# Optimization experiments

Measured on AMD Instinct MI355X. Metric: run time of the kernel, lower is better.

Reference implementation:

```python
import jax, jax.numpy as jnp
import numpy as np

N_NODES = 100000
N_EDGES = 3200000
IN_DIM = 512
HID_DIM = 16
OUT_DIM = 64


def _gcn_layer(E, X, W, b, n_nodes):
    # Standard GCN layer (CatGNN GCNLayer_MPNN_2):
    # add self-loops, symmetric deg^-1/2 normalization, project, gather-scatter sum.
    src = jnp.concatenate([E[0], jnp.arange(n_nodes, dtype=E.dtype)])
    dst = jnp.concatenate([E[1], jnp.arange(n_nodes, dtype=E.dtype)])
    deg = jax.ops.segment_sum(jnp.ones_like(dst, dtype=X.dtype), dst, num_segments=n_nodes)
    dinv = jnp.where(deg > 0, jax.lax.rsqrt(deg), 0.0)  # deg^-1/2, safe
    h = X @ W  # [N, d_out] project BEFORE aggregation (cheaper gather)
    norm = dinv[src] * dinv[dst]  # [E+N]
    msg = h[src] * norm[:, None]  # gather + scale
    out = jax.ops.segment_sum(msg, dst, num_segments=n_nodes)  # scatter-sum
    return out + b


def setup_inputs() -> dict:
    key = jax.random.key(0)
    k1, k2, k3, k4, k5 = jax.random.split(key, 5)
    V = jnp.arange(N_NODES, dtype=jnp.int64)
    E = jax.random.randint(k1, (2, N_EDGES), 0, N_NODES, dtype=jnp.int64)
    X = jax.random.normal(k2, (N_NODES, IN_DIM), dtype=jnp.float32)
    # Glorot-style init for layer weights
    W1 = jax.random.normal(k3, (IN_DIM, HID_DIM), dtype=jnp.float32) / np.sqrt(IN_DIM)
    b1 = jnp.zeros((HID_DIM,), dtype=jnp.float32)
    W2 = jax.random.normal(k4, (HID_DIM, OUT_DIM), dtype=jnp.float32) / np.sqrt(HID_DIM)
    b2 = jnp.zeros((OUT_DIM,), dtype=jnp.float32)
    return {"V": V, "E": E, "X": X, "W1": W1, "b1": b1, "W2": W2, "b2": b2}


def reference(V, E, X, W1, b1, W2, b2):
    n_nodes = V.shape[0]
    H = jax.nn.relu(_gcn_layer(E, X, W1, b1, n_nodes))
    # dropout is identity in eval mode
    H = _gcn_layer(E, H, W2, b2, n_nodes)
    return H
```

## Files before the change

kernel.cpp:

```cpp
#include <hip/hip_runtime.h>

#define HID 16
#define ODIM 64
#define IDIM 512
#define BKB 8
#define BKS 256
#define PTILE 4096
#define MAXBE 12288

__global__ __launch_bounds__(256) void k_bhist(const int* __restrict__ dst,
                                               int* __restrict__ bcnt, int ne, int nbk) {
    __shared__ int h[512];
    for (int t = threadIdx.x; t < 512; t += 256) h[t] = 0;
    __syncthreads();
    int stride = gridDim.x * blockDim.x;
    for (int e = blockIdx.x * blockDim.x + threadIdx.x; e < ne; e += stride)
        atomicAdd(&h[dst[e] >> BKB], 1);
    __syncthreads();
    for (int t = threadIdx.x; t < nbk; t += 256)
        if (h[t]) atomicAdd(&bcnt[t], h[t]);
}

__global__ __launch_bounds__(512) void k_bscan(const int* __restrict__ bcnt,
                                               int* __restrict__ bbase,
                                               int* __restrict__ bcur, int nbk) {
    __shared__ int s[512];
    int t = threadIdx.x;
    int v = (t < nbk) ? bcnt[t] : 0;
    s[t] = v;
    __syncthreads();
    for (int off = 1; off < 512; off <<= 1) {
        int u = (t >= off) ? s[t - off] : 0;
        __syncthreads();
        s[t] += u;
        __syncthreads();
    }
    if (t < nbk) { int b = s[t] - v; bbase[t] = b; bcur[t] = b; }
}

__global__ __launch_bounds__(512) void k_part(const int* __restrict__ src,
                                              const int* __restrict__ dst,
                                              int* __restrict__ bcur,
                                              unsigned int* __restrict__ ebuf,
                                              int ne, int nbk) {
    __shared__ int h[512], sc[512], base[512], lcur[512];
    __shared__ unsigned int sval[PTILE];
    __shared__ int saddr[PTILE];
    int e0 = blockIdx.x * PTILE;
    int m = ne - e0; if (m > PTILE) m = PTILE;
    if (m <= 0) return;
    int t = threadIdx.x;
    h[t] = 0;
    __syncthreads();
    for (int k = t; k < m; k += 512) atomicAdd(&h[dst[e0 + k] >> BKB], 1);
    __syncthreads();
    int hv = h[t];
    sc[t] = hv;
    __syncthreads();
    for (int off = 1; off < 512; off <<= 1) {
        int u = (t >= off) ? sc[t - off] : 0;
        __syncthreads();
        sc[t] += u;
        __syncthreads();
    }
    base[t] = hv ? atomicAdd(&bcur[t], hv) : 0;
    lcur[t] = 0;
    __syncthreads();
    for (int k = t; k < m; k += 512) {
        int d = dst[e0 + k];
        int b = d >> BKB;
        int r = atomicAdd(&lcur[b], 1);
        int slot = sc[b] - h[b] + r;
        sval[slot] = ((unsigned int)src[e0 + k] << BKB) | (unsigned int)(d & (BKS - 1));
        saddr[slot] = base[b] + r;
    }
    __syncthreads();
    for (int k = t; k < m; k += 512) ebuf[saddr[k]] = sval[k];
}

__global__ __launch_bounds__(256) void k_csr(const int* __restrict__ bbase,
                                             const int* __restrict__ bcnt,
                                             const unsigned int* __restrict__ ebuf,
                                             int* __restrict__ cnt,
                                             int* __restrict__ row_start,
                                             int* __restrict__ csr_src, int n) {
    __shared__ int h[256], sc[256], lc[256];
    __shared__ int stage[MAXBE];
    int bk = blockIdx.x;
    int node0 = bk << BKB;
    int ebase = bbase[bk];
    int ecnt = bcnt[bk];
    int t = threadIdx.x;
    h[t] = 0; lc[t] = 0;
    __syncthreads();
    for (int k = t; k < ecnt; k += 256) atomicAdd(&h[ebuf[ebase + k] & (BKS - 1)], 1);
    __syncthreads();
    int hv = h[t];
    sc[t] = hv;
    __syncthreads();
    for (int off = 1; off < 256; off <<= 1) {
        int u = (t >= off) ? sc[t - off] : 0;
        __syncthreads();
        sc[t] += u;
        __syncthreads();
    }
    int node = node0 + t;
    if (node < n) { cnt[node] = hv; row_start[node] = ebase + sc[t] - hv; }
    if (ecnt <= MAXBE) {
        for (int k = t; k < ecnt; k += 256) {
            unsigned int p = ebuf[ebase + k];
            int dl = p & (BKS - 1);
            int r = atomicAdd(&lc[dl], 1);
            stage[sc[dl] - h[dl] + r] = (int)(p >> BKB);
        }
        __syncthreads();
        for (int k = t; k < ecnt; k += 256) csr_src[ebase + k] = stage[k];
    } else {
        for (int k = t; k < ecnt; k += 256) {
            unsigned int p = ebuf[ebase + k];
            int dl = p & (BKS - 1);
            int r = atomicAdd(&lc[dl], 1);
            csr_src[ebase + sc[dl] - h[dl] + r] = (int)(p >> BKB);
        }
    }
}

__global__ __launch_bounds__(256) void k_proj1(const float* __restrict__ X,
                                               const float* __restrict__ W1,
                                               const int* __restrict__ cnt,
                                               float* __restrict__ hs1, int n) {
    __shared__ float Ws[IDIM * HID];
    for (int t = threadIdx.x; t < IDIM * HID; t += 256) Ws[t] = W1[t];
    __syncthreads();

    int i = blockIdx.x * blockDim.x + threadIdx.x;
    if (i >= n) return;

    const float4* xr = (const float4*)(X + (size_t)i * IDIM);
    float acc[HID];
#pragma unroll
    for (int j = 0; j < HID; ++j) acc[j] = 0.f;

    for (int k4 = 0; k4 < IDIM / 4; ++k4) {
        float4 x = xr[k4];
        const float* w = &Ws[k4 * 4 * HID];
#pragma unroll
        for (int j = 0; j < HID; ++j) acc[j] += x.x * w[j];
#pragma unroll
        for (int j = 0; j < HID; ++j) acc[j] += x.y * w[HID + j];
#pragma unroll
        for (int j = 0; j < HID; ++j) acc[j] += x.z * w[2 * HID + j];
#pragma unroll
        for (int j = 0; j < HID; ++j) acc[j] += x.w * w[3 * HID + j];
    }

    float di = rsqrtf((float)(cnt[i] + 1));
    float4* h4 = (float4*)(hs1 + (size_t)i * HID);
#pragma unroll
    for (int q = 0; q < 4; ++q) {
        float4 v;
        v.x = acc[q * 4 + 0] * di;
        v.y = acc[q * 4 + 1] * di;
        v.z = acc[q * 4 + 2] * di;
        v.w = acc[q * 4 + 3] * di;
        h4[q] = v;
    }
}

__global__ __launch_bounds__(256) void k_gather(const int* __restrict__ row_start,
                                                const int* __restrict__ cnt,
                                                const int* __restrict__ csr_src,
                                                const float* __restrict__ hs,
                                                float* __restrict__ agg, int n) {
    int tid = blockIdx.x * blockDim.x + threadIdx.x;
    int i = tid >> 2;
    int q = tid & 3;
    if (i >= n) return;
    int rs = row_start[i];
    int c = cnt[i];
    const float4* h4 = (const float4*)hs;
    float4 acc = h4[(size_t)i * 4 + q];
    int k = 0;
    for (; k + 1 < c; k += 2) {
        int s0 = csr_src[rs + k];
        int s1 = csr_src[rs + k + 1];
        float4 v0 = h4[(size_t)s0 * 4 + q];
        float4 v1 = h4[(size_t)s1 * 4 + q];
        acc.x += v0.x; acc.y += v0.y; acc.z += v0.z; acc.w += v0.w;
        acc.x += v1.x; acc.y += v1.y; acc.z += v1.z; acc.w += v1.w;
    }
    if (k < c) {
        int s0 = csr_src[rs + k];
        float4 v0 = h4[(size_t)s0 * 4 + q];
        acc.x += v0.x; acc.y += v0.y; acc.z += v0.z; acc.w += v0.w;
    }
    ((float4*)agg)[(size_t)i * 4 + q] = acc;
}

__global__ void k_mid(const int* __restrict__ cnt, const float* __restrict__ b1,
                      float* __restrict__ buf, int n) {
    int t = blockIdx.x * blockDim.x + threadIdx.x;
    if (t >= n * HID) return;
    int i = t >> 4;
    int j = t & 15;
    float di = rsqrtf((float)(cnt[i] + 1));
    float h = di * buf[t] + b1[j];
    h = fmaxf(h, 0.f);
    buf[t] = h * di;
}

__global__ __launch_bounds__(256) void k_out(const int* __restrict__ cnt,
                                             const float* __restrict__ agg2,
                                             const float* __restrict__ W2,
                                             const float* __restrict__ b2,
                                             float* __restrict__ out, int n) {
    __shared__ float Ws[HID * ODIM];
    __shared__ float bs[ODIM];
    for (int t = threadIdx.x; t < HID * ODIM; t += 256) Ws[t] = W2[t];
    if (threadIdx.x < ODIM) bs[threadIdx.x] = b2[threadIdx.x];
    __syncthreads();

    int t = blockIdx.x * blockDim.x + threadIdx.x;
    if (t >= n * ODIM) return;
    int i = t >> 6;
    int j = t & 63;
    float di = rsqrtf((float)(cnt[i] + 1));
    const float* g = agg2 + (size_t)i * HID;
    float acc = 0.f;
#pragma unroll
    for (int k = 0; k < HID; ++k) acc += g[k] * Ws[k * ODIM + j];
    out[t] = di * acc + bs[j];
}

extern "C" void kernel_launch(void* const* d_in, const int* in_sizes, int n_in,
                              void* d_out, int out_size, void* d_ws, size_t ws_size,
                              hipStream_t stream) {
    const int* E = (const int*)d_in[1];
    const float* X = (const float*)d_in[2];
    const float* W1 = (const float*)d_in[3];
    const float* b1 = (const float*)d_in[4];
    const float* W2 = (const float*)d_in[5];
    const float* b2 = (const float*)d_in[6];
    float* out = (float*)d_out;

    const int n = in_sizes[0];
    const int ne = in_sizes[1] / 2;
    const int* src = E;
    const int* dst = E + ne;
    const int nbk = (n + BKS - 1) >> BKB;

    char* ws = (char*)d_ws;
    int* bcnt = (int*)ws;
    int* bbase = (int*)(ws + (8u << 10));
    int* bcur = (int*)(ws + (16u << 10));
    int* cnt = (int*)(ws + (1u << 20));
    int* row_start = (int*)(ws + (2u << 20));
    unsigned int* ebuf = (unsigned int*)(ws + (3u << 20));
    float* B1 = (float*)(ws + (3u << 20));
    float* B2 = (float*)(ws + (10u << 20));
    int* csr_src = (int*)(ws + (17u << 20));

    hipMemsetAsync(bcnt, 0, nbk * sizeof(int), stream);
    k_bhist<<<1024, 256, 0, stream>>>(dst, bcnt, ne, nbk);
    k_bscan<<<1, 512, 0, stream>>>(bcnt, bbase, bcur, nbk);
    k_part<<<(ne + PTILE - 1) / PTILE, 512, 0, stream>>>(src, dst, bcur, ebuf, ne, nbk);
    k_csr<<<nbk, 256, 0, stream>>>(bbase, bcnt, ebuf, cnt, row_start, csr_src, n);

    k_proj1<<<(n + 255) / 256, 256, 0, stream>>>(X, W1, cnt, B1, n);
    k_gather<<<(n * 4 + 255) / 256, 256, 0, stream>>>(row_start, cnt, csr_src, B1, B2, n);
    k_mid<<<(n * HID + 255) / 256, 256, 0, stream>>>(cnt, b1, B2, n);
    k_gather<<<(n * 4 + 255) / 256, 256, 0, stream>>>(row_start, cnt, csr_src, B2, B1, n);
    k_out<<<(n * ODIM + 255) / 256, 256, 0, stream>>>(cnt, B1, W2, b2, out, n);
}
```

Baseline: 555.9 us.

## Drop CSR build; aggregate per bucket with LDS atomics and fuse epilogues

Removes the per-bucket CSR sort and instead computes only degrees, then aggregates each 256-node destination bucket directly from the bucketed edge buffer into shared memory using float atomics. The ReLU/bias/normalization step is fused into the first aggregation, and the W2 projection plus bias into the second. This eliminates the csr_src build and several separate elementwise kernels. The cost is heavy LDS atomic contention with nondeterministic summation order, and only about 391 blocks of 512 threads, which limits parallelism.

```diff
diff --git a/kernel.cpp b/kernel.cpp
--- a/kernel.cpp
+++ b/kernel.cpp
@@ -6,7 +6,6 @@
 #define BKB 8
 #define BKS 256
 #define PTILE 4096
-#define MAXBE 12288
 
 __global__ __launch_bounds__(256) void k_bhist(const int* __restrict__ dst,
                                                int* __restrict__ bcnt, int ne, int nbk) {
@@ -78,56 +77,25 @@
     for (int k = t; k < m; k += 512) ebuf[saddr[k]] = sval[k];
 }
 
-__global__ __launch_bounds__(256) void k_csr(const int* __restrict__ bbase,
+__global__ __launch_bounds__(256) void k_deg(const int* __restrict__ bbase,
                                              const int* __restrict__ bcnt,
                                              const unsigned int* __restrict__ ebuf,
-                                             int* __restrict__ cnt,
-                                             int* __restrict__ row_start,
-                                             int* __restrict__ csr_src, int n) {
-    __shared__ int h[256], sc[256], lc[256];
-    __shared__ int stage[MAXBE];
+                                             float* __restrict__ dinv, int n) {
+    __shared__ int h[BKS];
     int bk = blockIdx.x;
-    int node0 = bk << BKB;
-    int ebase = bbase[bk];
-    int ecnt = bcnt[bk];
-    int t = threadIdx.x;
-    h[t] = 0; lc[t] = 0;
-    __syncthreads();
-    for (int k = t; k < ecnt; k += 256) atomicAdd(&h[ebuf[ebase + k] & (BKS - 1)], 1);
-    __syncthreads();
-    int hv = h[t];
-    sc[t] = hv;
-    __syncthreads();
-    for (int off = 1; off < 256; off <<= 1) {
-        int u = (t >= off) ? sc[t - off] : 0;
-        __syncthreads();
-        sc[t] += u;
-        __syncthreads();
-    }
-    int node = node0 + t;
-    if (node < n) { cnt[node] = hv; row_start[node] = ebase + sc[t] - hv; }
-    if (ecnt <= MAXBE) {
-        for (int k = t; k < ecnt; k += 256) {
-            unsigned int p = ebuf[ebase + k];
-            int dl = p & (BKS - 1);
-            int r = atomicAdd(&lc[dl], 1);
-            stage[sc[dl] - h[dl] + r] = (int)(p >> BKB);
-        }
-        __syncthreads();
-        for (int k = t; k < ecnt; k += 256) csr_src[ebase + k] = stage[k];
-    } else {
-        for (int k = t; k < ecnt; k += 256) {
-            unsigned int p = ebuf[ebase + k];
-            int dl = p & (BKS - 1);
-            int r = atomicAdd(&lc[dl], 1);
-            csr_src[ebase + sc[dl] - h[dl] + r] = (int)(p >> BKB);
-        }
-    }
+    int t = threadIdx.x;
+    h[t] = 0;
+    __syncthreads();
+    int eb = bbase[bk], ec = bcnt[bk];
+    for (int k = t; k < ec; k += 256) atomicAdd(&h[ebuf[eb + k] & (BKS - 1)], 1);
+    __syncthreads();
+    int node = (bk << BKB) + t;
+    if (node < n) dinv[node] = rsqrtf((float)(h[t] + 1));
 }
 
 __global__ __launch_bounds__(256) void k_proj1(const float* __restrict__ X,
                                                const float* __restrict__ W1,
-                                               const int* __restrict__ cnt,
+                                               const float* __restrict__ dinv,
                                                float* __restrict__ hs1, int n) {
     __shared__ float Ws[IDIM * HID];
     for (int t = threadIdx.x; t < IDIM * HID; t += 256) Ws[t] = W1[t];
@@ -154,7 +122,7 @@
         for (int j = 0; j < HID; ++j) acc[j] += x.w * w[3 * HID + j];
     }
 
-    float di = rsqrtf((float)(cnt[i] + 1));
+    float di = dinv[i];
     float4* h4 = (float4*)(hs1 + (size_t)i * HID);
 #pragma unroll
     for (int q = 0; q < 4; ++q) {
@@ -167,69 +135,100 @@
     }
 }
 
-__global__ __launch_bounds__(256) void k_gather(const int* __restrict__ row_start,
-                                                const int* __restrict__ cnt,
-                                                const int* __restrict__ csr_src,
-                                                const float* __restrict__ hs,
-                                                float* __restrict__ agg, int n) {
-    int tid = blockIdx.x * blockDim.x + threadIdx.x;
-    int i = tid >> 2;
-    int q = tid & 3;
-    if (i >= n) return;
-    int rs = row_start[i];
-    int c = cnt[i];
-    const float4* h4 = (const float4*)hs;
-    float4 acc = h4[(size_t)i * 4 + q];
-    int k = 0;
-    for (; k + 1 < c; k += 2) {
-        int s0 = csr_src[rs + k];
-        int s1 = csr_src[rs + k + 1];
-        float4 v0 = h4[(size_t)s0 * 4 + q];
-        float4 v1 = h4[(size_t)s1 * 4 + q];
-        acc.x += v0.x; acc.y += v0.y; acc.z += v0.z; acc.w += v0.w;
-        acc.x += v1.x; acc.y += v1.y; acc.z += v1.z; acc.w += v1.w;
-    }
-    if (k < c) {
-        int s0 = csr_src[rs + k];
-        float4 v0 = h4[(size_t)s0 * 4 + q];
-        acc.x += v0.x; acc.y += v0.y; acc.z += v0.z; acc.w += v0.w;
-    }
-    ((float4*)agg)[(size_t)i * 4 + q] = acc;
-}
-
-__global__ void k_mid(const int* __restrict__ cnt, const float* __restrict__ b1,
-                      float* __restrict__ buf, int n) {
-    int t = blockIdx.x * blockDim.x + threadIdx.x;
-    if (t >= n * HID) return;
-    int i = t >> 4;
-    int j = t & 15;
-    float di = rsqrtf((float)(cnt[i] + 1));
-    float h = di * buf[t] + b1[j];
-    h = fmaxf(h, 0.f);
-    buf[t] = h * di;
-}
-
-__global__ __launch_bounds__(256) void k_out(const int* __restrict__ cnt,
-                                             const float* __restrict__ agg2,
-                                             const float* __restrict__ W2,
-                                             const float* __restrict__ b2,
-                                             float* __restrict__ out, int n) {
+__global__ __launch_bounds__(512) void k_gagg1(const int* __restrict__ bbase,
+                                               const int* __restrict__ bcnt,
+                                               const unsigned int* __restrict__ ebuf,
+                                               const float* __restrict__ hs,
+                                               const float* __restrict__ dinv,
+                                               const float* __restrict__ b1,
+                                               float* __restrict__ hs2, int n) {
+    __shared__ float acc[BKS * 17];
+    int t = threadIdx.x;
+    int bk = blockIdx.x;
+    int node0 = bk << BKB;
+    for (int idx = t; idx < BKS * HID; idx += 512) {
+        int nd = idx >> 4, j = idx & 15;
+        int g = node0 + nd;
+        acc[nd * 17 + j] = (g < n) ? hs[(size_t)g * HID + j] : 0.f;
+    }
+    __syncthreads();
+    int eb = bbase[bk], ec = bcnt[bk];
+    int q = t & 3;
+    for (int k = t >> 2; k < ec; k += 128) {
+        unsigned int p = ebuf[eb + k];
+        int dl = p & (BKS - 1);
+        int s = p >> BKB;
+        float4 v = ((const float4*)hs)[(size_t)s * 4 + q];
+        float* a = &acc[dl * 17 + q * 4];
+        atomicAdd(a + 0, v.x);
+        atomicAdd(a + 1, v.y);
+        atomicAdd(a + 2, v.z);
+        atomicAdd(a + 3, v.w);
+    }
+    __syncthreads();
+    for (int idx = t; idx < BKS * HID; idx += 512) {
+        int nd = idx >> 4, j = idx & 15;
+        int g = node0 + nd;
+        if (g >= n) continue;
+        float dv = dinv[g];
+        float h = fmaxf(dv * acc[nd * 17 + j] + b1[j], 0.f);
+        hs2[(size_t)g * HID + j] = h * dv;
+    }
+}
+
+__global__ __launch_bounds__(512) void k_gagg2(const int* __restrict__ bbase,
+                                               const int* __restrict__ bcnt,
+                                               const unsigned int* __restrict__ ebuf,
+                                               const float* __restrict__ hs,
+                                               const float* __restrict__ dinv,
+                                               const float* __restrict__ W2,
+                                               const float* __restrict__ b2,
+                                               float* __restrict__ out, int n) {
+    __shared__ float acc[BKS * 17];
     __shared__ float Ws[HID * ODIM];
     __shared__ float bs[ODIM];
-    for (int t = threadIdx.x; t < HID * ODIM; t += 256) Ws[t] = W2[t];
-    if (threadIdx.x < ODIM) bs[threadIdx.x] = b2[threadIdx.x];
-    __syncthreads();
-
-    int t = blockIdx.x * blockDim.x + threadIdx.x;
-    if (t >= n * ODIM) return;
-    int i = t >> 6;
-    int j = t & 63;
-    float di = rsqrtf((float)(cnt[i] + 1));
-    const float* g = agg2 + (size_t)i * HID;
-    float acc = 0.f;
-#pragma unroll
-    for (int k = 0; k < HID; ++k) acc += g[k] * Ws[k * ODIM + j];
-    out[t] = di * acc + bs[j];
+    __shared__ float dv[BKS];
+    int t = threadIdx.x;
+    int bk = blockIdx.x;
+    int node0 = bk << BKB;
+    for (int idx = t; idx < HID * ODIM; idx += 512) Ws[idx] = W2[idx];
+    if (t < ODIM) bs[t] = b2[t];
+    for (int idx = t; idx < BKS * HID; idx += 512) {
+        int nd = idx >> 4, j = idx & 15;
+        int g = node0 + nd;
+        acc[nd * 17 + j] = (g < n) ? hs[(size_t)g * HID + j] : 0.f;
+    }
+    if (t < BKS) {
+        int g = node0 + t;
+        dv[t] = (g < n) ? dinv[g] : 0.f;
+    }
+    __syncthreads();
+    int eb = bbase[bk], ec = bcnt[bk];
+    int q = t & 3;
+    for (int k = t >> 2; k < ec; k += 128) {
+        unsigned int p = ebuf[eb + k];
+        int dl = p & (BKS - 1);
+        int s = p >> BKB;
+        float4 v = ((const float4*)hs)[(size_t)s * 4 + q];
+        float* a = &acc[dl * 17 + q * 4];
+        atomicAdd(a + 0, v.x);
+        atomicAdd(a + 1, v.y);
+        atomicAdd(a + 2, v.z);
+        atomicAdd(a + 3, v.w);
+    }
+    __syncthreads();
+    int o = t & 63;
+    int nsub = t >> 6;
+    for (int it = 0; it < 32; ++it) {
+        int nd = it * 8 + nsub;
+        int g = node0 + nd;
+        if (g >= n) continue;
+        const float* arow = &acc[nd * 17];
+        float s_ = 0.f;
+#pragma unroll
+        for (int k = 0; k < HID; ++k) s_ += arow[k] * Ws[k * ODIM + o];
+        out[(size_t)g * ODIM + o] = dv[nd] * s_ + bs[o];
+    }
 }
 
 extern "C" void kernel_launch(void* const* d_in, const int* in_sizes, int n_in,
@@ -253,22 +252,18 @@
     int* bcnt = (int*)ws;
     int* bbase = (int*)(ws + (8u << 10));
     int* bcur = (int*)(ws + (16u << 10));
-    int* cnt = (int*)(ws + (1u << 20));
-    int* row_start = (int*)(ws + (2u << 20));
-    unsigned int* ebuf = (unsigned int*)(ws + (3u << 20));
-    float* B1 = (float*)(ws + (3u << 20));
-    float* B2 = (float*)(ws + (10u << 20));
-    int* csr_src = (int*)(ws + (17u << 20));
+    float* dinv = (float*)(ws + (1u << 20));
+    unsigned int* ebuf = (unsigned int*)(ws + (2u << 20));
+    float* B1 = (float*)(ws + (15u << 20));
+    float* B2 = (float*)(ws + (22u << 20));
 
     hipMemsetAsync(bcnt, 0, nbk * sizeof(int), stream);
     k_bhist<<<1024, 256, 0, stream>>>(dst, bcnt, ne, nbk);
     k_bscan<<<1, 512, 0, stream>>>(bcnt, bbase, bcur, nbk);
     k_part<<<(ne + PTILE - 1) / PTILE, 512, 0, stream>>>(src, dst, bcur, ebuf, ne, nbk);
-    k_csr<<<nbk, 256, 0, stream>>>(bbase, bcnt, ebuf, cnt, row_start, csr_src, n);
-
-    k_proj1<<<(n + 255) / 256, 256, 0, stream>>>(X, W1, cnt, B1, n);
-    k_gather<<<(n * 4 + 255) / 256, 256, 0, stream>>>(row_start, cnt, csr_src, B1, B2, n);
-    k_mid<<<(n * HID + 255) / 256, 256, 0, stream>>>(cnt, b1, B2, n);
-    k_gather<<<(n * 4 + 255) / 256, 256, 0, stream>>>(row_start, cnt, csr_src, B2, B1, n);
-    k_out<<<(n * ODIM + 255) / 256, 256, 0, stream>>>(cnt, B1, W2, b2, out, n);
-}
+    k_deg<<<nbk, 256, 0, stream>>>(bbase, bcnt, ebuf, dinv, n);
+
+    k_proj1<<<(n + 255) / 256, 256, 0, stream>>>(X, W1, dinv, B1, n);
+    k_gagg1<<<nbk, 512, 0, stream>>>(bbase, bcnt, ebuf, B1, dinv, b1, B2, n);
+    k_gagg2<<<nbk, 512, 0, stream>>>(bbase, bcnt, ebuf, B2, dinv, W2, b2, out, n);
+}
```

Result: slower. 1.112 ms (+100.0%).
